# Kernel tuning notes

Hardware: AMD Instinct MI355X
Metric: run time of the kernel (lower is better)

Reference implementation:

```python
import jax, jax.numpy as jnp
import numpy as np

LOWER_T = 6.0
UPPER_T = 50.0


def _conv(x, w, pad_h, pad_w):
    # x: [N,1,H,W] or [N,Cin,H,W]; w: [O,I,kh,kw]; cross-correlation like torch Conv2d
    return jax.lax.conv_general_dilated(
        x, w, window_strides=(1, 1),
        padding=[(pad_h, pad_h), (pad_w, pad_w)],
        dimension_numbers=('NCHW', 'OIHW', 'NCHW'))


def setup_inputs() -> dict:
    key = jax.random.key(0)
    H = W = 4096
    img = jax.random.uniform(key, (1, 3, H, W), dtype=jnp.float32) * 255.0

    # scipy.signal.gaussian(5, std=1.0), unnormalized window
    std = 1.0
    g = np.exp(-0.5 * ((np.arange(5, dtype=np.float32) - 2.0) / std) ** 2).astype(np.float32)
    gauss = jnp.asarray(g)  # [5]

    sobel = jnp.asarray(np.array([[1, 0, -1], [2, 0, -2], [1, 0, -1]], dtype=np.float32))  # [3,3]

    f = np.zeros((8, 1, 3, 3), dtype=np.float32)
    f[:, 0, 1, 1] = 1.0
    offs = [(1, 2), (2, 2), (2, 1), (2, 0), (1, 0), (0, 0), (0, 1), (0, 2)]  # 0,45,...,315 deg
    for k, (r, c) in enumerate(offs):
        f[k, 0, r, c] = -1.0
    dir_w = jnp.asarray(f)  # [8,1,3,3]

    return {"img": img, "gauss": gauss, "sobel": sobel, "dir_w": dir_w}


def reference(img, gauss, sobel, dir_w):
    N, C, H, W = img.shape  # N == 1, C == 3
    x = img.reshape(C, 1, H, W)  # treat channels as batch

    # separable gaussian blur: 1x5 then 5x1, padding 2 (matches torch Conv2d)
    gw_h = gauss.reshape(1, 1, 1, 5)
    gw_v = gauss.reshape(1, 1, 5, 1)
    blurred = _conv(_conv(x, gw_h, 0, 2), gw_v, 2, 0)  # [3,1,H,W]

    sw_h = sobel.reshape(1, 1, 3, 3)
    sw_v = sobel.T.reshape(1, 1, 3, 3)
    gx = _conv(blurred, sw_h, 1, 1)  # [3,1,H,W]
    gy = _conv(blurred, sw_v, 1, 1)

    # per-channel magnitude summed over RGB -> [1,1,H,W]
    grad_mag = jnp.sqrt(gx * gx + gy * gy + 1e-8).sum(axis=0, keepdims=True)[:, 0:1]

    gx_sum = gx.sum(axis=0, keepdims=True)[:, 0:1]
    gy_sum = gy.sum(axis=0, keepdims=True)[:, 0:1]
    ori = jnp.arctan2(gy_sum, gx_sum) * (180.0 / 3.14159) + 180.0
    ori = jnp.round(ori / 45.0) * 45.0

    all_filtered = _conv(grad_mag, dir_w, 1, 1)  # [1,8,H,W]

    idx_pos = jnp.mod(ori / 45.0, 8.0).astype(jnp.int32)          # [1,1,H,W]
    idx_neg = jnp.mod(ori / 45.0 + 4.0, 8.0).astype(jnp.int32)

    cs_pos = jnp.take_along_axis(all_filtered, idx_pos, axis=1)  # [1,1,H,W]
    cs_neg = jnp.take_along_axis(all_filtered, idx_neg, axis=1)

    is_max = jnp.minimum(cs_pos, cs_neg) > 0.0

    thin = jnp.where(is_max, grad_mag, 0.0)
    keep = is_max & (thin >= LOWER_T) & (thin <= UPPER_T)
    thresholded = jnp.where(keep, 1.0, 0.0).astype(jnp.float32)  # [1,1,H,W]
    return thresholded
```

## Files before the change

### kernel.cpp

```cpp
#include <hip/hip_runtime.h>


#define IMG_H 4096
#define IMG_W 4096

constexpr int TW = 32, TH = 32;
constexpr int HBH = 40, HBW = 40;
constexpr int BH  = 36, BW  = 40;
constexpr int MH  = 34, MW  = 36;

template<bool INTERIOR>
__device__ __forceinline__ void pipeline(
    const float* __restrict__ img,
    float g0, float g1, float g2, float g3, float g4,
    int X0, int Y0, int tid,
    float* __restrict__ s_hb, float* __restrict__ s_bl,
    float* __restrict__ s_bs, float* __restrict__ s_mg,
    float* __restrict__ out) {

  for (int ch = 0; ch < 3; ++ch) {
    const float* im = img + (size_t)ch * ((size_t)IMG_H * IMG_W);

    for (int j = tid; j < HBH * 10; j += 256) {
      int r = j / 10, g = j - r * 10;
      int c0 = g * 4;
      int gy = Y0 - 4 + r;
      float4 o;
      if (INTERIOR) {
        const float* row = im + (size_t)gy * IMG_W + (X0 - 4 + c0);
        float4 va = *(const float4*)(row);
        float4 vb = *(const float4*)(row + 4);
        o.x = g0 * va.x + g1 * va.y + g2 * va.z + g3 * va.w + g4 * vb.x;
        o.y = g0 * va.y + g1 * va.z + g2 * va.w + g3 * vb.x + g4 * vb.y;
        o.z = g0 * va.z + g1 * va.w + g2 * vb.x + g3 * vb.y + g4 * vb.z;
        o.w = g0 * va.w + g1 * vb.x + g2 * vb.y + g3 * vb.z + g4 * vb.w;
      } else if ((unsigned)gy < IMG_H) {
        int cb = X0 - 4 + c0;
        const float* row = im + (size_t)gy * IMG_W;
        float a0, a1, a2, a3, a4, a5, a6, a7;
        if (cb >= 0 && cb + 7 < IMG_W) {
          float4 va = *(const float4*)(row + cb);
          float4 vb = *(const float4*)(row + cb + 4);
          a0 = va.x; a1 = va.y; a2 = va.z; a3 = va.w;
          a4 = vb.x; a5 = vb.y; a6 = vb.z; a7 = vb.w;
        } else {
          float t[8];
#pragma unroll
          for (int u = 0; u < 8; ++u) {
            int x = cb + u;
            t[u] = ((unsigned)x < IMG_W) ? row[x] : 0.f;
          }
          a0 = t[0]; a1 = t[1]; a2 = t[2]; a3 = t[3];
          a4 = t[4]; a5 = t[5]; a6 = t[6]; a7 = t[7];
        }
        o.x = g0 * a0 + g1 * a1 + g2 * a2 + g3 * a3 + g4 * a4;
        o.y = g0 * a1 + g1 * a2 + g2 * a3 + g3 * a4 + g4 * a5;
        o.z = g0 * a2 + g1 * a3 + g2 * a4 + g3 * a5 + g4 * a6;
        o.w = g0 * a3 + g1 * a4 + g2 * a5 + g3 * a6 + g4 * a7;
      } else {
        o = make_float4(0.f, 0.f, 0.f, 0.f);
      }
      *(float4*)&s_hb[r * HBW + c0] = o;
    }
    __syncthreads();

    for (int j = tid; j < BH * 10; j += 256) {
      int r = j / 10, g = j - r * 10;
      int c0 = g * 4;
      const float* p = &s_hb[r * HBW + c0];
      float4 a0 = *(const float4*)(p);
      float4 a1 = *(const float4*)(p + HBW);
      float4 a2 = *(const float4*)(p + 2 * HBW);
      float4 a3 = *(const float4*)(p + 3 * HBW);
      float4 a4 = *(const float4*)(p + 4 * HBW);
      float4 v;
      v.x = g0 * a0.x + g1 * a1.x + g2 * a2.x + g3 * a3.x + g4 * a4.x;
      v.y = g0 * a0.y + g1 * a1.y + g2 * a2.y + g3 * a3.y + g4 * a4.y;
      v.z = g0 * a0.z + g1 * a1.z + g2 * a2.z + g3 * a3.z + g4 * a4.z;
      v.w = g0 * a0.w + g1 * a1.w + g2 * a2.w + g3 * a3.w + g4 * a4.w;
      if (!INTERIOR) {
        int gy = Y0 - 2 + r;
        bool rok = (unsigned)gy < IMG_H;
        int gx0 = X0 - 2 + c0;
        v.x = (rok && (unsigned)(gx0    ) < IMG_W) ? v.x : 0.f;
        v.y = (rok && (unsigned)(gx0 + 1) < IMG_W) ? v.y : 0.f;
        v.z = (rok && (unsigned)(gx0 + 2) < IMG_W) ? v.z : 0.f;
        v.w = (rok && (unsigned)(gx0 + 3) < IMG_W) ? v.w : 0.f;
      }
      *(float4*)&s_bl[r * BW + c0] = v;
      float4* ps = (float4*)&s_bs[r * BW + c0];
      if (ch == 0) {
        *ps = v;
      } else {
        float4 s = *ps;
        s.x += v.x; s.y += v.y; s.z += v.z; s.w += v.w;
        *ps = s;
      }
    }
    __syncthreads();

    for (int j = tid; j < MH * 9; j += 256) {
      int r = j / 9, g = j - r * 9;
      int c0 = g * 4;
      float w0[6], w1[6], w2[6];
      const float* p = &s_bl[r * BW + c0];
      { float4 a = *(const float4*)(p);          float2 b = *(const float2*)(p + 4);
        w0[0]=a.x; w0[1]=a.y; w0[2]=a.z; w0[3]=a.w; w0[4]=b.x; w0[5]=b.y; }
      { float4 a = *(const float4*)(p + BW);     float2 b = *(const float2*)(p + BW + 4);
        w1[0]=a.x; w1[1]=a.y; w1[2]=a.z; w1[3]=a.w; w1[4]=b.x; w1[5]=b.y; }
      { float4 a = *(const float4*)(p + 2 * BW); float2 b = *(const float2*)(p + 2 * BW + 4);
        w2[0]=a.x; w2[1]=a.y; w2[2]=a.z; w2[3]=a.w; w2[4]=b.x; w2[5]=b.y; }
      float res[4];
#pragma unroll
      for (int e = 0; e < 4; ++e) {
        float gxv = w0[e] - w0[e + 2] + 2.f * w1[e] - 2.f * w1[e + 2] + w2[e] - w2[e + 2];
        float gyv = w0[e] + 2.f * w0[e + 1] + w0[e + 2] - w2[e] - 2.f * w2[e + 1] - w2[e + 2];
        float m = sqrtf(gxv * gxv + gyv * gyv + 1e-8f);
        if (!INTERIOR) {
          int gy = Y0 - 1 + r;
          int gx = X0 - 1 + c0 + e;
          m = ((unsigned)gy < IMG_H && (unsigned)gx < IMG_W) ? m : 0.f;
        }
        res[e] = m;
      }
      float4* pd = (float4*)&s_mg[r * MW + c0];
      if (ch == 0) {
        *pd = make_float4(res[0], res[1], res[2], res[3]);
      } else {
        float4 s = *pd;
        s.x += res[0]; s.y += res[1]; s.z += res[2]; s.w += res[3];
        *pd = s;
      }
    }
    __syncthreads();
  }

  {
    const int ty  = tid >> 3;
    const int tx0 = (tid & 7) << 2;
    const int row1 = (ty + 1) * MW;

    float4 q0 = *(const float4*)&s_mg[row1 + tx0];
    float4 q1 = *(const float4*)&s_mg[row1 + tx0 + 4];
    float mcs[4];
    mcs[0] = q0.y; mcs[1] = q0.z; mcs[2] = q0.w; mcs[3] = q1.x;

    bool band = false;
#pragma unroll
    for (int e = 0; e < 4; ++e)
      band = band || (mcs[e] >= 6.0f && mcs[e] <= 50.0f);

    float4 resv = make_float4(0.f, 0.f, 0.f, 0.f);
    if (__ballot(band) != 0ULL) {
      float w0[8], w1[8], w2[8];
#pragma unroll
      for (int rr = 0; rr < 3; ++rr) {
        float* w = (rr == 0) ? w0 : (rr == 1) ? w1 : w2;
        float4 p = *(const float4*)&s_bs[(ty + 1 + rr) * BW + tx0];
        float4 q = *(const float4*)&s_bs[(ty + 1 + rr) * BW + tx0 + 4];
        w[0]=p.x; w[1]=p.y; w[2]=p.z; w[3]=p.w; w[4]=q.x; w[5]=q.y; w[6]=q.z; w[7]=q.w;
      }
      const unsigned long long off_tbl = 0xDDDCDBFF23242501ULL;
      float res[4];
#pragma unroll
      for (int e = 0; e < 4; ++e) {
        int tx = tx0 + e;
        float b00 = w0[e + 1], b01 = w0[e + 2], b02 = w0[e + 3];
        float b10 = w1[e + 1],                  b12 = w1[e + 3];
        float b20 = w2[e + 1], b21 = w2[e + 2], b22 = w2[e + 3];
        float gxs = b00 - b02 + 2.f * b10 - 2.f * b12 + b20 - b22;
        float gys = b00 + 2.f * b01 + b02 - b20 - 2.f * b21 - b22;
        float ax = fabsf(gxs), ay = fabsf(gys);
        float f1 = ay - 0.41421356f * ax;
        float f2 = ay - 2.4142137f * ax;
        int off;
        if (fminf(fabsf(f1), fabsf(f2)) < 1e-4f * (ax + ay)) {
          float ori = atan2f(gys, gxs) * 57.295827908797776f + 180.0f;
          int k = (int)rintf(ori / 45.0f);
          int ip = k & 7;
          off = (int)(signed char)(off_tbl >> (ip * 8));
        } else {
          off = (f1 <= 0.f) ? 1
              : (f2 >= 0.f) ? MW
              : (((__float_as_uint(gxs) ^ __float_as_uint(gys)) >> 31) ? (MW - 1)
                                                                       : (MW + 1));
        }
        int ctr = row1 + (tx + 1);
        float mc  = mcs[e];
        float csp = mc - s_mg[ctr + off];
        float csn = mc - s_mg[ctr - off];
        bool is_max = fminf(csp, csn) > 0.0f;
        bool keep = is_max && (mc >= 6.0f) && (mc <= 50.0f);
        res[e] = keep ? 1.0f : 0.0f;
      }
      resv = make_float4(res[0], res[1], res[2], res[3]);
    }
    *(float4*)&out[(size_t)(Y0 + ty) * IMG_W + (X0 + tx0)] = resv;
  }
}

__global__ __launch_bounds__(256, 6)
void canny_fused(const float* __restrict__ img,
                 const float* __restrict__ gauss,
                 float* __restrict__ out) {
  __shared__ float s_hb[HBH * HBW];
  __shared__ float s_bl[BH * BW];
  __shared__ float s_bs[BH * BW];
  __shared__ float s_mg[MH * MW];

  const int tid = threadIdx.x;
  const int X0 = blockIdx.x * TW;
  const int Y0 = blockIdx.y * TH;
  const float g0 = gauss[0], g1 = gauss[1], g2 = gauss[2],
              g3 = gauss[3], g4 = gauss[4];

  const bool interior = (blockIdx.x >= 1) && (blockIdx.x <= 126) &&
                        (blockIdx.y >= 1) && (blockIdx.y <= 126);
  if (interior)
    pipeline<true >(img, g0, g1, g2, g3, g4, X0, Y0, tid, s_hb, s_bl, s_bs, s_mg, out);
  else
    pipeline<false>(img, g0, g1, g2, g3, g4, X0, Y0, tid, s_hb, s_bl, s_bs, s_mg, out);
}

extern "C" void kernel_launch(void* const* d_in, const int* in_sizes, int n_in,
                              void* d_out, int out_size, void* d_ws, size_t ws_size,
                              hipStream_t stream) {
  const float* img   = (const float*)d_in[0];
  const float* gauss = (const float*)d_in[1];
  float* out = (float*)d_out;
  dim3 grid(IMG_W / TW, IMG_H / TH);
  canny_fused<<<grid, 256, 0, stream>>>(img, gauss, out);
}
```

Baseline: 341.6 us.

## Prefetch next channel's image rows during Sobel stage and pad LDS rows

For interior tiles, global loads for the next channel's horizontal-blur input are issued into registers before the Sobel/magnitude stage and stored to shared memory afterwards, overlapping DRAM latency with compute. Shared-memory row pitch of the blur buffers is padded from 40 to 44 floats to reduce bank conflicts. The boundary path is split into a separate non-inlined function. Holding prefetched data in registers raises register pressure and may lower occupancy.

Measured after the change: 336.9 us. About the same (-1.4%).

```diff
diff --git a/kernel.cpp b/kernel.cpp
--- a/kernel.cpp
+++ b/kernel.cpp
@@ -5,12 +5,76 @@
 #define IMG_W 4096
 
 constexpr int TW = 32, TH = 32;
-constexpr int HBH = 40, HBW = 40;
-constexpr int BH  = 36, BW  = 40;
+constexpr int HBH = 40, HBW = 44;
+constexpr int BH  = 36, BW  = 44;
 constexpr int MH  = 34, MW  = 36;
 
-template<bool INTERIOR>
-__device__ __forceinline__ void pipeline(
+__device__ __forceinline__ void stageD(
+    const float* __restrict__ s_bs, const float* __restrict__ s_mg,
+    float* __restrict__ out, int X0, int Y0, int tid) {
+  const int ty  = tid >> 3;
+  const int tx0 = (tid & 7) << 2;
+  const int row1 = (ty + 1) * MW;
+
+  float4 q0 = *(const float4*)&s_mg[row1 + tx0];
+  float4 q1 = *(const float4*)&s_mg[row1 + tx0 + 4];
+  float mcs[4];
+  mcs[0] = q0.y; mcs[1] = q0.z; mcs[2] = q0.w; mcs[3] = q1.x;
+
+  bool band = false;
+#pragma unroll
+  for (int e = 0; e < 4; ++e)
+    band = band || (mcs[e] >= 6.0f && mcs[e] <= 50.0f);
+
+  float4 resv = make_float4(0.f, 0.f, 0.f, 0.f);
+  if (__ballot(band) != 0ULL) {
+    float w0[8], w1[8], w2[8];
+#pragma unroll
+    for (int rr = 0; rr < 3; ++rr) {
+      float* w = (rr == 0) ? w0 : (rr == 1) ? w1 : w2;
+      float4 p = *(const float4*)&s_bs[(ty + 1 + rr) * BW + tx0];
+      float4 q = *(const float4*)&s_bs[(ty + 1 + rr) * BW + tx0 + 4];
+      w[0]=p.x; w[1]=p.y; w[2]=p.z; w[3]=p.w; w[4]=q.x; w[5]=q.y; w[6]=q.z; w[7]=q.w;
+    }
+    const unsigned long long off_tbl = 0xDDDCDBFF23242501ULL;
+    float res[4];
+#pragma unroll
+    for (int e = 0; e < 4; ++e) {
+      int tx = tx0 + e;
+      float b00 = w0[e + 1], b01 = w0[e + 2], b02 = w0[e + 3];
+      float b10 = w1[e + 1],                  b12 = w1[e + 3];
+      float b20 = w2[e + 1], b21 = w2[e + 2], b22 = w2[e + 3];
+      float gxs = b00 - b02 + 2.f * b10 - 2.f * b12 + b20 - b22;
+      float gys = b00 + 2.f * b01 + b02 - b20 - 2.f * b21 - b22;
+      float ax = fabsf(gxs), ay = fabsf(gys);
+      float f1 = ay - 0.41421356f * ax;
+      float f2 = ay - 2.4142137f * ax;
+      int off;
+      if (fminf(fabsf(f1), fabsf(f2)) < 1e-4f * (ax + ay)) {
+        float ori = atan2f(gys, gxs) * 57.295827908797776f + 180.0f;
+        int k = (int)rintf(ori / 45.0f);
+        int ip = k & 7;
+        off = (int)(signed char)(off_tbl >> (ip * 8));
+      } else {
+        off = (f1 <= 0.f) ? 1
+            : (f2 >= 0.f) ? MW
+            : (((__float_as_uint(gxs) ^ __float_as_uint(gys)) >> 31) ? (MW - 1)
+                                                                     : (MW + 1));
+      }
+      int ctr = row1 + (tx + 1);
+      float mc  = mcs[e];
+      float csp = mc - s_mg[ctr + off];
+      float csn = mc - s_mg[ctr - off];
+      bool is_max = fminf(csp, csn) > 0.0f;
+      bool keep = is_max && (mc >= 6.0f) && (mc <= 50.0f);
+      res[e] = keep ? 1.0f : 0.0f;
+    }
+    resv = make_float4(res[0], res[1], res[2], res[3]);
+  }
+  *(float4*)&out[(size_t)(Y0 + ty) * IMG_W + (X0 + tx0)] = resv;
+}
+
+__device__ __forceinline__ void pipeline_interior(
     const float* __restrict__ img,
     float g0, float g1, float g2, float g3, float g4,
     int X0, int Y0, int tid,
@@ -18,6 +82,117 @@
     float* __restrict__ s_bs, float* __restrict__ s_mg,
     float* __restrict__ out) {
 
+  const int rA0 = tid / 10, cA0 = (tid - rA0 * 10) * 4;
+  const int jA1 = tid + 256;
+  const int rA1 = jA1 / 10, cA1 = (jA1 - rA1 * 10) * 4;
+  const bool hasA1 = (tid < 144);
+
+  float4 pa0, pb0, pa1, pb1;
+
+  auto issueA = [&](int ch) {
+    const float* im = img + (size_t)ch * ((size_t)IMG_H * IMG_W);
+    const float* r0 = im + (size_t)(Y0 - 4 + rA0) * IMG_W + (X0 - 4 + cA0);
+    pa0 = *(const float4*)r0;
+    pb0 = *(const float4*)(r0 + 4);
+    if (hasA1) {
+      const float* r1 = im + (size_t)(Y0 - 4 + rA1) * IMG_W + (X0 - 4 + cA1);
+      pa1 = *(const float4*)r1;
+      pb1 = *(const float4*)(r1 + 4);
+    }
+  };
+  auto storeA = [&]() {
+    auto h5 = [&](const float4& a, const float4& b) {
+      float4 o;
+      o.x = g0 * a.x + g1 * a.y + g2 * a.z + g3 * a.w + g4 * b.x;
+      o.y = g0 * a.y + g1 * a.z + g2 * a.w + g3 * b.x + g4 * b.y;
+      o.z = g0 * a.z + g1 * a.w + g2 * b.x + g3 * b.y + g4 * b.z;
+      o.w = g0 * a.w + g1 * b.x + g2 * b.y + g3 * b.z + g4 * b.w;
+      return o;
+    };
+    *(float4*)&s_hb[rA0 * HBW + cA0] = h5(pa0, pb0);
+    if (hasA1) *(float4*)&s_hb[rA1 * HBW + cA1] = h5(pa1, pb1);
+  };
+
+  auto stageB = [&](int ch) {
+    for (int j = tid; j < BH * 10; j += 256) {
+      int r = j / 10, g = j - r * 10;
+      int c0 = g * 4;
+      const float* p = &s_hb[r * HBW + c0];
+      float4 a0 = *(const float4*)(p);
+      float4 a1 = *(const float4*)(p + HBW);
+      float4 a2 = *(const float4*)(p + 2 * HBW);
+      float4 a3 = *(const float4*)(p + 3 * HBW);
+      float4 a4 = *(const float4*)(p + 4 * HBW);
+      float4 v;
+      v.x = g0 * a0.x + g1 * a1.x + g2 * a2.x + g3 * a3.x + g4 * a4.x;
+      v.y = g0 * a0.y + g1 * a1.y + g2 * a2.y + g3 * a3.y + g4 * a4.y;
+      v.z = g0 * a0.z + g1 * a1.z + g2 * a2.z + g3 * a3.z + g4 * a4.z;
+      v.w = g0 * a0.w + g1 * a1.w + g2 * a2.w + g3 * a3.w + g4 * a4.w;
+      *(float4*)&s_bl[r * BW + c0] = v;
+      float4* ps = (float4*)&s_bs[r * BW + c0];
+      if (ch == 0) {
+        *ps = v;
+      } else {
+        float4 s = *ps;
+        s.x += v.x; s.y += v.y; s.z += v.z; s.w += v.w;
+        *ps = s;
+      }
+    }
+  };
+
+  auto stageC = [&](int ch) {
+    for (int j = tid; j < MH * 9; j += 256) {
+      int r = j / 9, g = j - r * 9;
+      int c0 = g * 4;
+      float w0[6], w1[6], w2[6];
+      const float* p = &s_bl[r * BW + c0];
+      { float4 a = *(const float4*)(p);          float2 b = *(const float2*)(p + 4);
+        w0[0]=a.x; w0[1]=a.y; w0[2]=a.z; w0[3]=a.w; w0[4]=b.x; w0[5]=b.y; }
+      { float4 a = *(const float4*)(p + BW);     float2 b = *(const float2*)(p + BW + 4);
+        w1[0]=a.x; w1[1]=a.y; w1[2]=a.z; w1[3]=a.w; w1[4]=b.x; w1[5]=b.y; }
+      { float4 a = *(const float4*)(p + 2 * BW); float2 b = *(const float2*)(p + 2 * BW + 4);
+        w2[0]=a.x; w2[1]=a.y; w2[2]=a.z; w2[3]=a.w; w2[4]=b.x; w2[5]=b.y; }
+      float res[4];
+#pragma unroll
+      for (int e = 0; e < 4; ++e) {
+        float gxv = w0[e] - w0[e + 2] + 2.f * w1[e] - 2.f * w1[e + 2] + w2[e] - w2[e + 2];
+        float gyv = w0[e] + 2.f * w0[e + 1] + w0[e + 2] - w2[e] - 2.f * w2[e + 1] - w2[e + 2];
+        res[e] = sqrtf(gxv * gxv + gyv * gyv + 1e-8f);
+      }
+      float4* pd = (float4*)&s_mg[r * MW + c0];
+      if (ch == 0) {
+        *pd = make_float4(res[0], res[1], res[2], res[3]);
+      } else {
+        float4 s = *pd;
+        s.x += res[0]; s.y += res[1]; s.z += res[2]; s.w += res[3];
+        *pd = s;
+      }
+    }
+  };
+
+  issueA(0);
+  storeA();
+  __syncthreads();
+#pragma unroll
+  for (int ch = 0; ch < 3; ++ch) {
+    stageB(ch);
+    __syncthreads();
+    if (ch < 2) issueA(ch + 1);
+    stageC(ch);
+    if (ch < 2) storeA();
+    __syncthreads();
+  }
+  stageD(s_bs, s_mg, out, X0, Y0, tid);
+}
+
+__device__ void pipeline_boundary(
+    const float* __restrict__ img,
+    float g0, float g1, float g2, float g3, float g4,
+    int X0, int Y0, int tid,
+    float* __restrict__ s_hb, float* __restrict__ s_bl,
+    float* __restrict__ s_bs, float* __restrict__ s_mg,
+    float* __restrict__ out) {
+
   for (int ch = 0; ch < 3; ++ch) {
     const float* im = img + (size_t)ch * ((size_t)IMG_H * IMG_W);
 
@@ -26,15 +201,7 @@
       int c0 = g * 4;
       int gy = Y0 - 4 + r;
       float4 o;
-      if (INTERIOR) {
-        const float* row = im + (size_t)gy * IMG_W + (X0 - 4 + c0);
-        float4 va = *(const float4*)(row);
-        float4 vb = *(const float4*)(row + 4);
-        o.x = g0 * va.x + g1 * va.y + g2 * va.z + g3 * va.w + g4 * vb.x;
-        o.y = g0 * va.y + g1 * va.z + g2 * va.w + g3 * vb.x + g4 * vb.y;
-        o.z = g0 * va.z + g1 * va.w + g2 * vb.x + g3 * vb.y + g4 * vb.z;
-        o.w = g0 * va.w + g1 * vb.x + g2 * vb.y + g3 * vb.z + g4 * vb.w;
-      } else if ((unsigned)gy < IMG_H) {
+      if ((unsigned)gy < IMG_H) {
         int cb = X0 - 4 + c0;
         const float* row = im + (size_t)gy * IMG_W;
         float a0, a1, a2, a3, a4, a5, a6, a7;
@@ -78,7 +245,7 @@
       v.y = g0 * a0.y + g1 * a1.y + g2 * a2.y + g3 * a3.y + g4 * a4.y;
       v.z = g0 * a0.z + g1 * a1.z + g2 * a2.z + g3 * a3.z + g4 * a4.z;
       v.w = g0 * a0.w + g1 * a1.w + g2 * a2.w + g3 * a3.w + g4 * a4.w;
-      if (!INTERIOR) {
+      {
         int gy = Y0 - 2 + r;
         bool rok = (unsigned)gy < IMG_H;
         int gx0 = X0 - 2 + c0;
@@ -116,12 +283,9 @@
         float gxv = w0[e] - w0[e + 2] + 2.f * w1[e] - 2.f * w1[e + 2] + w2[e] - w2[e + 2];
         float gyv = w0[e] + 2.f * w0[e + 1] + w0[e + 2] - w2[e] - 2.f * w2[e + 1] - w2[e + 2];
         float m = sqrtf(gxv * gxv + gyv * gyv + 1e-8f);
-        if (!INTERIOR) {
-          int gy = Y0 - 1 + r;
-          int gx = X0 - 1 + c0 + e;
-          m = ((unsigned)gy < IMG_H && (unsigned)gx < IMG_W) ? m : 0.f;
-        }
-        res[e] = m;
+        int gy = Y0 - 1 + r;
+        int gx = X0 - 1 + c0 + e;
+        res[e] = ((unsigned)gy < IMG_H && (unsigned)gx < IMG_W) ? m : 0.f;
       }
       float4* pd = (float4*)&s_mg[r * MW + c0];
       if (ch == 0) {
@@ -134,69 +298,7 @@
     }
     __syncthreads();
   }
-
-  {
-    const int ty  = tid >> 3;
-    const int tx0 = (tid & 7) << 2;
-    const int row1 = (ty + 1) * MW;
-
-    float4 q0 = *(const float4*)&s_mg[row1 + tx0];
-    float4 q1 = *(const float4*)&s_mg[row1 + tx0 + 4];
-    float mcs[4];
-    mcs[0] = q0.y; mcs[1] = q0.z; mcs[2] = q0.w; mcs[3] = q1.x;
-
-    bool band = false;
-#pragma unroll
-    for (int e = 0; e < 4; ++e)
-      band = band || (mcs[e] >= 6.0f && mcs[e] <= 50.0f);
-
-    float4 resv = make_float4(0.f, 0.f, 0.f, 0.f);
-    if (__ballot(band) != 0ULL) {
-      float w0[8], w1[8], w2[8];
-#pragma unroll
-      for (int rr = 0; rr < 3; ++rr) {
-        float* w = (rr == 0) ? w0 : (rr == 1) ? w1 : w2;
-        float4 p = *(const float4*)&s_bs[(ty + 1 + rr) * BW + tx0];
-        float4 q = *(const float4*)&s_bs[(ty + 1 + rr) * BW + tx0 + 4];
-        w[0]=p.x; w[1]=p.y; w[2]=p.z; w[3]=p.w; w[4]=q.x; w[5]=q.y; w[6]=q.z; w[7]=q.w;
-      }
-      const unsigned long long off_tbl = 0xDDDCDBFF23242501ULL;
-      float res[4];
-#pragma unroll
-      for (int e = 0; e < 4; ++e) {
-        int tx = tx0 + e;
-        float b00 = w0[e + 1], b01 = w0[e + 2], b02 = w0[e + 3];
-        float b10 = w1[e + 1],                  b12 = w1[e + 3];
-        float b20 = w2[e + 1], b21 = w2[e + 2], b22 = w2[e + 3];
-        float gxs = b00 - b02 + 2.f * b10 - 2.f * b12 + b20 - b22;
-        float gys = b00 + 2.f * b01 + b02 - b20 - 2.f * b21 - b22;
-        float ax = fabsf(gxs), ay = fabsf(gys);
-        float f1 = ay - 0.41421356f * ax;
-        float f2 = ay - 2.4142137f * ax;
-        int off;
-        if (fminf(fabsf(f1), fabsf(f2)) < 1e-4f * (ax + ay)) {
-          float ori = atan2f(gys, gxs) * 57.295827908797776f + 180.0f;
-          int k = (int)rintf(ori / 45.0f);
-          int ip = k & 7;
-          off = (int)(signed char)(off_tbl >> (ip * 8));
-        } else {
-          off = (f1 <= 0.f) ? 1
-              : (f2 >= 0.f) ? MW
-              : (((__float_as_uint(gxs) ^ __float_as_uint(gys)) >> 31) ? (MW - 1)
-                                                                       : (MW + 1));
-        }
-        int ctr = row1 + (tx + 1);
-        float mc  = mcs[e];
-        float csp = mc - s_mg[ctr + off];
-        float csn = mc - s_mg[ctr - off];
-        bool is_max = fminf(csp, csn) > 0.0f;
-        bool keep = is_max && (mc >= 6.0f) && (mc <= 50.0f);
-        res[e] = keep ? 1.0f : 0.0f;
-      }
-      resv = make_float4(res[0], res[1], res[2], res[3]);
-    }
-    *(float4*)&out[(size_t)(Y0 + ty) * IMG_W + (X0 + tx0)] = resv;
-  }
+  stageD(s_bs, s_mg, out, X0, Y0, tid);
 }
 
 __global__ __launch_bounds__(256, 6)
@@ -217,9 +319,9 @@
   const bool interior = (blockIdx.x >= 1) && (blockIdx.x <= 126) &&
                         (blockIdx.y >= 1) && (blockIdx.y <= 126);
   if (interior)
-    pipeline<true >(img, g0, g1, g2, g3, g4, X0, Y0, tid, s_hb, s_bl, s_bs, s_mg, out);
+    pipeline_interior(img, g0, g1, g2, g3, g4, X0, Y0, tid, s_hb, s_bl, s_bs, s_mg, out);
   else
-    pipeline<false>(img, g0, g1, g2, g3, g4, X0, Y0, tid, s_hb, s_bl, s_bs, s_mg, out);
+    pipeline_boundary(img, g0, g1, g2, g3, g4, X0, Y0, tid, s_hb, s_bl, s_bs, s_mg, out);
 }
 
 extern "C" void kernel_launch(void* const* d_in, const int* in_sizes, int n_in,
```
